# Optimization experiments

Measured on AMD Instinct MI355X. Metric: run time of the kernel, lower is better.

## Reference

```python
import jax, jax.numpy as jnp
import numpy as np

H = 12        # heads
D = 768       # d_model
DK = D // H   # per-head dim
B, S = 1, 4096


def setup_inputs() -> dict:
    key = jax.random.key(0)
    ks = jax.random.split(key, 8)
    scale = 1.0 / np.sqrt(D)
    return {
        "q": jax.random.normal(ks[0], (B, S, D), jnp.float32),
        "k": jax.random.normal(ks[1], (B, S, D), jnp.float32),
        "v": jax.random.normal(ks[2], (B, S, D), jnp.float32),
        "Wq": jax.random.normal(ks[3], (D, D), jnp.float32) * scale,
        "bq": jnp.zeros((D,), jnp.float32),
        "Wk": jax.random.normal(ks[4], (D, D), jnp.float32) * scale,
        "bk": jnp.zeros((D,), jnp.float32),
        "Wv": jax.random.normal(ks[5], (D, D), jnp.float32) * scale,
        "bv": jnp.zeros((D,), jnp.float32),
        "Wo": jax.random.normal(ks[6], (D, D), jnp.float32) * scale,
        "bo": jnp.zeros((D,), jnp.float32),
    }


def reference(q, k, v, Wq, bq, Wk, bk, Wv, bv, Wo, bo):
    bs, sq, _ = q.shape
    sk = k.shape[1]
    # projections, then split heads: (b, h, s, dk)
    qh = (q @ Wq + bq).reshape(bs, sq, H, DK).transpose(0, 2, 1, 3)
    kh = (k @ Wk + bk).reshape(bs, sk, H, DK).transpose(0, 2, 1, 3)
    vh = (v @ Wv + bv).reshape(bs, sk, H, DK).transpose(0, 2, 1, 3)
    # scaled dot-product attention (mask=None, dropout inactive)
    scores = jnp.einsum("bhqd,bhkd->bhqk", qh, kh) / jnp.sqrt(jnp.float32(DK))
    attn = jax.nn.softmax(scores, axis=-1)
    ctx = jnp.einsum("bhqk,bhkd->bhqd", attn, vh)
    concat = ctx.transpose(0, 2, 1, 3).reshape(bs, sq, D)
    return concat @ Wo + bo
```

## Files before the change

### kernel.cpp

```cpp
#include <hip/hip_runtime.h>
#include <hip/hip_bf16.h>


constexpr int S_LEN = 4096;
constexpr int D_MODEL = 768;
constexpr int N_HEADS = 12;
constexpr int D_HEAD = 64;
constexpr int SEG = 2;
constexpr int SEG_LEN = S_LEN / SEG;

#define QSCALE 0.180336880111120f

typedef _Float16 f16;
typedef __attribute__((ext_vector_type(8))) _Float16 f16x8;
typedef __attribute__((ext_vector_type(4))) _Float16 f16x4;
typedef __attribute__((ext_vector_type(4))) float f32x4;

__global__ __launch_bounds__(256) void prep_kernel(
    const float* __restrict__ q, const float* __restrict__ k,
    const float* __restrict__ v, f16* __restrict__ qh,
    f16* __restrict__ kh, f16* __restrict__ vh,
    const float* __restrict__ W0, const float* __restrict__ W1,
    const float* __restrict__ W2, const float* __restrict__ W3,
    f16* __restrict__ WtBase)
{
    __shared__ float T[64][65];
    int bid = blockIdx.x;
    const int t = threadIdx.x;
    if (bid < 4608) {
        int g = bid / 1536, r = bid % 1536;
        const float* x = (g == 0) ? q : (g == 1) ? k : v;
        f16* y = (g == 0) ? qh : (g == 1) ? kh : vh;
        int i = (r * 256 + t) * 8;
        float4 a = *(const float4*)&x[i];
        float4 b = *(const float4*)&x[i + 4];
        f16x8 h = { (f16)a.x, (f16)a.y, (f16)a.z, (f16)a.w,
                    (f16)b.x, (f16)b.y, (f16)b.z, (f16)b.w };
        *(f16x8*)&y[i] = h;
        return;
    }
    bid -= 4608;
    int g = bid / 144, r = bid % 144;
    const float* W = (g == 0) ? W0 : (g == 1) ? W1 : (g == 2) ? W2 : W3;
    f16* Wt = WtBase + (size_t)g * D_MODEL * D_MODEL;
    const int r0 = (r / 12) * 64;
    const int c0 = (r % 12) * 64;
    #pragma unroll
    for (int i = 0; i < 16; ++i) {
        int e = t + 256 * i; int rr = e >> 6, cc = e & 63;
        T[rr][cc] = W[(size_t)(r0 + rr) * D_MODEL + c0 + cc];
    }
    __syncthreads();
    #pragma unroll
    for (int i = 0; i < 16; ++i) {
        int e = t + 256 * i; int rr = e >> 6, cc = e & 63;
        Wt[(size_t)(c0 + rr) * D_MODEL + r0 + cc] = (f16)T[cc][rr];
    }
}

#define GSTR 72

__device__ __forceinline__ void gemm128_core(
    const f16* __restrict__ A, const f16* __restrict__ B,
    f16* As, f16* Bs, int K, int row0, int col0, int t, f32x4 acc[4][4])
{
    const int w = t >> 6, l = t & 63, quad = l >> 4, l15 = l & 15;
    const int wm = (w & 1) * 64, wn = (w >> 1) * 64;

    f16x8 pa[4], pb[4];
    #pragma unroll
    for (int i = 0; i < 4; ++i) {
        int idx = i * 256 + t;
        int r = idx >> 3, c = (idx & 7) * 8;
        pa[i] = *(const f16x8*)&A[(size_t)(row0 + r) * K + c];
        pb[i] = *(const f16x8*)&B[(size_t)(col0 + r) * K + c];
    }

    for (int k0 = 0; k0 < K; k0 += 64) {
        __syncthreads();
        #pragma unroll
        for (int i = 0; i < 4; ++i) {
            int idx = i * 256 + t;
            int r = idx >> 3, c = (idx & 7) * 8;
            *(f16x8*)&As[r * GSTR + c] = pa[i];
            *(f16x8*)&Bs[r * GSTR + c] = pb[i];
        }
        __syncthreads();

        int kn = k0 + 64;
        if (kn < K) {
            #pragma unroll
            for (int i = 0; i < 4; ++i) {
                int idx = i * 256 + t;
                int r = idx >> 3, c = (idx & 7) * 8;
                pa[i] = *(const f16x8*)&A[(size_t)(row0 + r) * K + kn + c];
                pb[i] = *(const f16x8*)&B[(size_t)(col0 + r) * K + kn + c];
            }
        }

        #pragma unroll
        for (int kc = 0; kc < 2; ++kc) {
            f16x8 af[4], bf[4];
            #pragma unroll
            for (int mt = 0; mt < 4; ++mt)
                af[mt] = *(f16x8*)&As[(wm + mt * 16 + l15) * GSTR + kc * 32 + quad * 8];
            #pragma unroll
            for (int nt = 0; nt < 4; ++nt)
                bf[nt] = *(f16x8*)&Bs[(wn + nt * 16 + l15) * GSTR + kc * 32 + quad * 8];
            #pragma unroll
            for (int mt = 0; mt < 4; ++mt)
                #pragma unroll
                for (int nt = 0; nt < 4; ++nt)
                    acc[mt][nt] = __builtin_amdgcn_mfma_f32_16x16x32_f16(
                        af[mt], bf[nt], acc[mt][nt], 0, 0, 0);
        }
    }
}

__global__ __launch_bounds__(256) void qkv_gemm_kernel(
    const f16* __restrict__ qh, const f16* __restrict__ kh,
    const f16* __restrict__ vh, const f16* __restrict__ WtBase,
    const float* __restrict__ bq, const float* __restrict__ bk,
    const float* __restrict__ bv,
    f16* __restrict__ Qp, f16* __restrict__ Kp, f16* __restrict__ Vpt)
{
    __shared__ f16 As[128 * GSTR];
    __shared__ f16 Bs[128 * GSTR];
    const size_t DD = (size_t)D_MODEL * D_MODEL;
    int bid = blockIdx.x;
    int g = bid / 192, r = bid % 192;

    const f16 *A, *B; const float* bias; f16* Y;
    int N; bool biasRow; float scale;
    int row0, col0;
    if (g == 0) {
        A = qh; B = WtBase; bias = bq; Y = Qp;
        N = D_MODEL; biasRow = false; scale = QSCALE;
        row0 = (r / 6) * 128; col0 = (r % 6) * 128;
    } else if (g == 1) {
        A = kh; B = WtBase + DD; bias = bk; Y = Kp;
        N = D_MODEL; biasRow = false; scale = 1.0f;
        row0 = (r / 6) * 128; col0 = (r % 6) * 128;
    } else {
        A = WtBase + 2 * DD; B = vh; bias = bv; Y = Vpt;
        N = S_LEN; biasRow = true; scale = 1.0f;
        row0 = (r / 32) * 128; col0 = (r % 32) * 128;
    }

    f32x4 acc[4][4];
    #pragma unroll
    for (int i = 0; i < 4; ++i)
        #pragma unroll
        for (int j = 0; j < 4; ++j) acc[i][j] = (f32x4){0.f, 0.f, 0.f, 0.f};

    const int t = threadIdx.x;
    gemm128_core(A, B, As, Bs, D_MODEL, row0, col0, t, acc);

    const int w = t >> 6, l = t & 63, quad = l >> 4, l15 = l & 15;
    const int wm = (w & 1) * 64, wn = (w >> 1) * 64;
    #pragma unroll
    for (int mt = 0; mt < 4; ++mt) {
        #pragma unroll
        for (int nt = 0; nt < 4; ++nt) {
            int col = col0 + wn + nt * 16 + l15;
            #pragma unroll
            for (int reg = 0; reg < 4; ++reg) {
                int row = row0 + wm + mt * 16 + quad * 4 + reg;
                float b = biasRow ? bias[row] : bias[col];
                Y[(size_t)row * N + col] = (f16)((acc[mt][nt][reg] + b) * scale);
            }
        }
    }
}

#define LSTR 72

__global__ __launch_bounds__(256, 4) void flash_attn_part_kernel(
    const f16* __restrict__ Q, const f16* __restrict__ K,
    const f16* __restrict__ Vg, f16* __restrict__ Opart,
    float* __restrict__ lsum)
{
    __shared__ f16 Ks[64 * LSTR];
    __shared__ f16 Vt[64 * LSTR];

    const int t    = threadIdx.x;
    const int w    = t >> 6;
    const int l    = t & 63;
    const int quad = l >> 4;
    const int l15  = l & 15;
    const int h    = blockIdx.y;
    const int q0   = blockIdx.x * 128;
    const int seg  = blockIdx.z;
    const int c0   = h * D_HEAD;
    const size_t SD = (size_t)S_LEN * D_MODEL;

    f16x8 qa[2][2];
    #pragma unroll
    for (int qt = 0; qt < 2; ++qt) {
        const f16* qrow = Q + (size_t)(q0 + w * 32 + qt * 16 + l15) * D_MODEL + c0;
        qa[qt][0] = *(const f16x8*)&qrow[quad * 8];
        qa[qt][1] = *(const f16x8*)&qrow[32 + quad * 8];
    }

    f32x4 ctx[2][4];
    float lAcc[2] = {0.f, 0.f};
    #pragma unroll
    for (int qt = 0; qt < 2; ++qt)
        #pragma unroll
        for (int i = 0; i < 4; ++i) ctx[qt][i] = (f32x4){0.f, 0.f, 0.f, 0.f};

    const int kt0 = seg * SEG_LEN;

    f16x8 kreg[2], vreg[2];
    #pragma unroll
    for (int i = 0; i < 2; ++i) {
        int idx = i * 256 + t;
        int r = idx >> 3, c = (idx & 7) * 8;
        kreg[i] = *(const f16x8*)&K[(size_t)(kt0 + r) * D_MODEL + c0 + c];
        vreg[i] = *(const f16x8*)&Vg[(size_t)(c0 + r) * S_LEN + kt0 + c];
    }

    for (int kt = kt0; kt < kt0 + SEG_LEN; kt += 64) {
        __syncthreads();
        #pragma unroll
        for (int i = 0; i < 2; ++i) {
            int idx = i * 256 + t;
            int r = idx >> 3, c = (idx & 7) * 8;
            *(f16x8*)&Ks[r * LSTR + c] = kreg[i];
            *(f16x8*)&Vt[r * LSTR + c] = vreg[i];
        }
        __syncthreads();

        int ktn = kt + 64;
        if (ktn < kt0 + SEG_LEN) {
            #pragma unroll
            for (int i = 0; i < 2; ++i) {
                int idx = i * 256 + t;
                int r = idx >> 3, c = (idx & 7) * 8;
                kreg[i] = *(const f16x8*)&K[(size_t)(ktn + r) * D_MODEL + c0 + c];
                vreg[i] = *(const f16x8*)&Vg[(size_t)(c0 + r) * S_LEN + ktn + c];
            }
        }

        f16x4 pfrag[2][4];
        #pragma unroll
        for (int nt = 0; nt < 4; ++nt) {
            f16x8 kb0 = *(f16x8*)&Ks[(nt * 16 + l15) * LSTR + quad * 8];
            f16x8 kb1 = *(f16x8*)&Ks[(nt * 16 + l15) * LSTR + 32 + quad * 8];
            #pragma unroll
            for (int qt = 0; qt < 2; ++qt) {
                f32x4 z = (f32x4){0.f, 0.f, 0.f, 0.f};
                z = __builtin_amdgcn_mfma_f32_16x16x32_f16(kb0, qa[qt][0], z, 0, 0, 0);
                z = __builtin_amdgcn_mfma_f32_16x16x32_f16(kb1, qa[qt][1], z, 0, 0, 0);
                float p0 = __builtin_amdgcn_exp2f(z[0]);
                float p1 = __builtin_amdgcn_exp2f(z[1]);
                float p2 = __builtin_amdgcn_exp2f(z[2]);
                float p3 = __builtin_amdgcn_exp2f(z[3]);
                lAcc[qt] += (p0 + p1) + (p2 + p3);
                pfrag[qt][nt] = (f16x4){ (f16)p0, (f16)p1, (f16)p2, (f16)p3 };
            }
        }

        #pragma unroll
        for (int mt = 0; mt < 4; ++mt) {
            #pragma unroll
            for (int nt = 0; nt < 4; ++nt) {
                f16x4 va = *(f16x4*)&Vt[(mt * 16 + l15) * LSTR + nt * 16 + quad * 4];
                #pragma unroll
                for (int qt = 0; qt < 2; ++qt)
                    ctx[qt][mt] = __builtin_amdgcn_mfma_f32_16x16x16f16(
                        va, pfrag[qt][nt], ctx[qt][mt], 0, 0, 0);
            }
        }
    }

    #pragma unroll
    for (int qt = 0; qt < 2; ++qt) {
        int qrow = q0 + w * 32 + qt * 16 + l15;
        #pragma unroll
        for (int mt = 0; mt < 4; ++mt) {
            f16x4 ov = { (f16)ctx[qt][mt][0], (f16)ctx[qt][mt][1],
                         (f16)ctx[qt][mt][2], (f16)ctx[qt][mt][3] };
            *(f16x4*)&Opart[(size_t)seg * SD + (size_t)qrow * D_MODEL
                            + c0 + mt * 16 + quad * 4] = ov;
        }
        float s = lAcc[qt];
        s += __shfl_xor(s, 16);
        s += __shfl_xor(s, 32);
        if (quad == 0)
            lsum[((size_t)seg * N_HEADS + h) * S_LEN + qrow] = s;
    }
}

__global__ __launch_bounds__(256) void combine_kernel(
    const f16* __restrict__ Opart, const float* __restrict__ lsum,
    f16* __restrict__ Ctx)
{
    const size_t SD = (size_t)S_LEN * D_MODEL;
    int tid = blockIdx.x * 256 + threadIdx.x;
    int idx = tid * 8;
    int row = idx / D_MODEL;
    int c   = idx % D_MODEL;
    int h   = c >> 6;
    float l0 = lsum[(size_t)h * S_LEN + row];
    float l1 = lsum[((size_t)N_HEADS + h) * S_LEN + row];
    float inv = 1.0f / (l0 + l1);
    f16x8 o0 = *(const f16x8*)&Opart[(size_t)row * D_MODEL + c];
    f16x8 o1 = *(const f16x8*)&Opart[SD + (size_t)row * D_MODEL + c];
    f16x8 r;
    #pragma unroll
    for (int j = 0; j < 8; ++j)
        r[j] = (f16)(((float)o0[j] + (float)o1[j]) * inv);
    *(f16x8*)&Ctx[(size_t)row * D_MODEL + c] = r;
}

__global__ __launch_bounds__(256) void oproj_kernel(
    const f16* __restrict__ Ctx, const f16* __restrict__ Wto,
    const float* __restrict__ bo, float* __restrict__ out)
{
    __shared__ f16 As[128 * GSTR];
    __shared__ f16 Bs[128 * GSTR];
    int bid = blockIdx.x;
    int row0 = (bid / 6) * 128, col0 = (bid % 6) * 128;

    f32x4 acc[4][4];
    #pragma unroll
    for (int i = 0; i < 4; ++i)
        #pragma unroll
        for (int j = 0; j < 4; ++j) acc[i][j] = (f32x4){0.f, 0.f, 0.f, 0.f};

    const int t = threadIdx.x;
    gemm128_core(Ctx, Wto, As, Bs, D_MODEL, row0, col0, t, acc);

    const int w = t >> 6, l = t & 63, quad = l >> 4, l15 = l & 15;
    const int wm = (w & 1) * 64, wn = (w >> 1) * 64;
    #pragma unroll
    for (int mt = 0; mt < 4; ++mt) {
        #pragma unroll
        for (int nt = 0; nt < 4; ++nt) {
            int col = col0 + wn + nt * 16 + l15;
            float b = bo[col];
            #pragma unroll
            for (int reg = 0; reg < 4; ++reg) {
                int row = row0 + wm + mt * 16 + quad * 4 + reg;
                out[(size_t)row * D_MODEL + col] = acc[mt][nt][reg] + b;
            }
        }
    }
}

extern "C" void kernel_launch(void* const* d_in, const int* in_sizes, int n_in,
                              void* d_out, int out_size, void* d_ws, size_t ws_size,
                              hipStream_t stream)
{
    const float* q  = (const float*)d_in[0];
    const float* k  = (const float*)d_in[1];
    const float* v  = (const float*)d_in[2];
    const float* Wq = (const float*)d_in[3];
    const float* bq = (const float*)d_in[4];
    const float* Wk = (const float*)d_in[5];
    const float* bk = (const float*)d_in[6];
    const float* Wv = (const float*)d_in[7];
    const float* bv = (const float*)d_in[8];
    const float* Wo = (const float*)d_in[9];
    const float* bo = (const float*)d_in[10];
    float* out = (float*)d_out;

    const size_t SD = (size_t)S_LEN * D_MODEL;
    const size_t DD = (size_t)D_MODEL * D_MODEL;
    f16* base   = (f16*)d_ws;
    f16* WtBase = base;
    f16* Wto    = WtBase + 3 * DD;
    f16* Qp     = base + 4 * DD;
    f16* Kp     = Qp + SD;
    f16* Vpt    = Kp + SD;
    f16* qh     = Vpt + SD;
    f16* kh     = qh + SD;
    f16* vh     = kh + SD;
    f16* Opart  = qh;
    f16* Ctx    = qh + 2 * SD;
    float* lsum = (float*)(base + 4 * DD + 6 * SD);

    prep_kernel<<<3 * 1536 + 4 * 144, 256, 0, stream>>>(
        q, k, v, qh, kh, vh, Wq, Wk, Wv, Wo, WtBase);

    qkv_gemm_kernel<<<3 * 192, 256, 0, stream>>>(
        qh, kh, vh, WtBase, bq, bk, bv, Qp, Kp, Vpt);

    dim3 gAttn(S_LEN / 128, N_HEADS, SEG);
    flash_attn_part_kernel<<<gAttn, 256, 0, stream>>>(Qp, Kp, Vpt, Opart, lsum);

    combine_kernel<<<1536, 256, 0, stream>>>(Opart, lsum, Ctx);

    oproj_kernel<<<192, 256, 0, stream>>>(Ctx, Wto, bo, out);
}
```

Before: 224.7 us.

## Load GEMM tiles directly to LDS with XOR swizzle instead of register staging

Changes the shared GEMM core used by the QKV and output projections. Tiles now go straight from global memory into LDS with global_load_lds, replacing the register prefetch followed by an LDS store. The padded row stride becomes a dense 64-wide layout with an XOR chunk swizzle to avoid bank conflicts. This frees registers and LDS space, but removes the software prefetch overlap: every iteration now waits on the load before its MFMAs run.

```diff
diff --git a/kernel.cpp b/kernel.cpp
--- a/kernel.cpp
+++ b/kernel.cpp
@@ -15,6 +15,13 @@
 typedef __attribute__((ext_vector_type(8))) _Float16 f16x8;
 typedef __attribute__((ext_vector_type(4))) _Float16 f16x4;
 typedef __attribute__((ext_vector_type(4))) float f32x4;
+
+__device__ __forceinline__ void cp16(const f16* gsrc, f16* ldsbase_uniform) {
+    __builtin_amdgcn_global_load_lds(
+        (__attribute__((address_space(1))) void*)(uintptr_t)gsrc,
+        (__attribute__((address_space(3))) void*)(uintptr_t)ldsbase_uniform,
+        16, 0, 0);
+}
 
 __global__ __launch_bounds__(256) void prep_kernel(
     const float* __restrict__ q, const float* __restrict__ k,
@@ -58,55 +65,38 @@
     }
 }
 
-#define GSTR 72
-
 __device__ __forceinline__ void gemm128_core(
     const f16* __restrict__ A, const f16* __restrict__ B,
     f16* As, f16* Bs, int K, int row0, int col0, int t, f32x4 acc[4][4])
 {
     const int w = t >> 6, l = t & 63, quad = l >> 4, l15 = l & 15;
     const int wm = (w & 1) * 64, wn = (w >> 1) * 64;
-
-    f16x8 pa[4], pb[4];
-    #pragma unroll
-    for (int i = 0; i < 4; ++i) {
-        int idx = i * 256 + t;
-        int r = idx >> 3, c = (idx & 7) * 8;
-        pa[i] = *(const f16x8*)&A[(size_t)(row0 + r) * K + c];
-        pb[i] = *(const f16x8*)&B[(size_t)(col0 + r) * K + c];
-    }
+    const int srow   = l >> 3;
+    const int gchunk = (l & 7) ^ srow;
+    const int swz    = l15 & 7;
 
     for (int k0 = 0; k0 < K; k0 += 64) {
         __syncthreads();
         #pragma unroll
-        for (int i = 0; i < 4; ++i) {
-            int idx = i * 256 + t;
-            int r = idx >> 3, c = (idx & 7) * 8;
-            *(f16x8*)&As[r * GSTR + c] = pa[i];
-            *(f16x8*)&Bs[r * GSTR + c] = pb[i];
+        for (int j = 0; j < 4; ++j) {
+            int m = w * 4 + j;
+            int r = m * 8 + srow;
+            cp16(&A[(size_t)(row0 + r) * K + k0 + gchunk * 8], &As[m * 512]);
+            cp16(&B[(size_t)(col0 + r) * K + k0 + gchunk * 8], &Bs[m * 512]);
         }
         __syncthreads();
-
-        int kn = k0 + 64;
-        if (kn < K) {
-            #pragma unroll
-            for (int i = 0; i < 4; ++i) {
-                int idx = i * 256 + t;
-                int r = idx >> 3, c = (idx & 7) * 8;
-                pa[i] = *(const f16x8*)&A[(size_t)(row0 + r) * K + kn + c];
-                pb[i] = *(const f16x8*)&B[(size_t)(col0 + r) * K + kn + c];
-            }
-        }
 
         #pragma unroll
         for (int kc = 0; kc < 2; ++kc) {
             f16x8 af[4], bf[4];
             #pragma unroll
             for (int mt = 0; mt < 4; ++mt)
-                af[mt] = *(f16x8*)&As[(wm + mt * 16 + l15) * GSTR + kc * 32 + quad * 8];
+                af[mt] = *(f16x8*)&As[(wm + mt * 16 + l15) * 64
+                                      + (((kc * 4 + quad) ^ swz) * 8)];
             #pragma unroll
             for (int nt = 0; nt < 4; ++nt)
-                bf[nt] = *(f16x8*)&Bs[(wn + nt * 16 + l15) * GSTR + kc * 32 + quad * 8];
+                bf[nt] = *(f16x8*)&Bs[(wn + nt * 16 + l15) * 64
+                                      + (((kc * 4 + quad) ^ swz) * 8)];
             #pragma unroll
             for (int mt = 0; mt < 4; ++mt)
                 #pragma unroll
@@ -124,8 +114,8 @@
     const float* __restrict__ bv,
     f16* __restrict__ Qp, f16* __restrict__ Kp, f16* __restrict__ Vpt)
 {
-    __shared__ f16 As[128 * GSTR];
-    __shared__ f16 Bs[128 * GSTR];
+    __shared__ f16 As[128 * 64];
+    __shared__ f16 Bs[128 * 64];
     const size_t DD = (size_t)D_MODEL * D_MODEL;
     int bid = blockIdx.x;
     int g = bid / 192, r = bid % 192;
@@ -318,8 +308,8 @@
     const f16* __restrict__ Ctx, const f16* __restrict__ Wto,
     const float* __restrict__ bo, float* __restrict__ out)
 {
-    __shared__ f16 As[128 * GSTR];
-    __shared__ f16 Bs[128 * GSTR];
+    __shared__ f16 As[128 * 64];
+    __shared__ f16 Bs[128 * 64];
     int bid = blockIdx.x;
     int row0 = (bid / 6) * 128, col0 = (bid % 6) * 128;
 
```

Measured after the change: 232.2 us. 1.03x slower.

## Split attention KV into four segments and halve GEMM N-tile width

Applied to the files above, without the earlier changes.

Raises the flash-attention KV split from 2 to 4 segments, so the grid has more blocks, and generalizes the combine kernel to sum an arbitrary number of partials. The QKV and output-projection GEMMs move from 128x128 to 128x64 tiles through a templated core, doubling block counts for better occupancy across the CUs. The workspace layout changes: Ctx now aliases Qp and lsum moves to make room for four Opart buffers. The trade-off is more partial-output traffic in combine and less operand reuse per GEMM tile.

```diff
diff --git a/kernel.cpp b/kernel.cpp
--- a/kernel.cpp
+++ b/kernel.cpp
@@ -6,7 +6,7 @@
 constexpr int D_MODEL = 768;
 constexpr int N_HEADS = 12;
 constexpr int D_HEAD = 64;
-constexpr int SEG = 2;
+constexpr int SEG = 4;
 constexpr int SEG_LEN = S_LEN / SEG;
 
 #define QSCALE 0.180336880111120f
@@ -60,19 +60,25 @@
 
 #define GSTR 72
 
-__device__ __forceinline__ void gemm128_core(
+template<int NT>
+__device__ __forceinline__ void gemm_core(
     const f16* __restrict__ A, const f16* __restrict__ B,
-    f16* As, f16* Bs, int K, int row0, int col0, int t, f32x4 acc[4][4])
+    f16* As, f16* Bs, int K, int row0, int col0, int t, f32x4 acc[4][NT])
 {
     const int w = t >> 6, l = t & 63, quad = l >> 4, l15 = l & 15;
-    const int wm = (w & 1) * 64, wn = (w >> 1) * 64;
-
-    f16x8 pa[4], pb[4];
+    const int wm = (w & 1) * 64, wn = (w >> 1) * 16 * NT;
+
+    f16x8 pa[4], pb[NT];
     #pragma unroll
     for (int i = 0; i < 4; ++i) {
         int idx = i * 256 + t;
         int r = idx >> 3, c = (idx & 7) * 8;
         pa[i] = *(const f16x8*)&A[(size_t)(row0 + r) * K + c];
+    }
+    #pragma unroll
+    for (int i = 0; i < NT; ++i) {
+        int idx = i * 256 + t;
+        int r = idx >> 3, c = (idx & 7) * 8;
         pb[i] = *(const f16x8*)&B[(size_t)(col0 + r) * K + c];
     }
 
@@ -83,6 +89,11 @@
             int idx = i * 256 + t;
             int r = idx >> 3, c = (idx & 7) * 8;
             *(f16x8*)&As[r * GSTR + c] = pa[i];
+        }
+        #pragma unroll
+        for (int i = 0; i < NT; ++i) {
+            int idx = i * 256 + t;
+            int r = idx >> 3, c = (idx & 7) * 8;
             *(f16x8*)&Bs[r * GSTR + c] = pb[i];
         }
         __syncthreads();
@@ -94,23 +105,28 @@
                 int idx = i * 256 + t;
                 int r = idx >> 3, c = (idx & 7) * 8;
                 pa[i] = *(const f16x8*)&A[(size_t)(row0 + r) * K + kn + c];
+            }
+            #pragma unroll
+            for (int i = 0; i < NT; ++i) {
+                int idx = i * 256 + t;
+                int r = idx >> 3, c = (idx & 7) * 8;
                 pb[i] = *(const f16x8*)&B[(size_t)(col0 + r) * K + kn + c];
             }
         }
 
         #pragma unroll
         for (int kc = 0; kc < 2; ++kc) {
-            f16x8 af[4], bf[4];
+            f16x8 af[4], bf[NT];
             #pragma unroll
             for (int mt = 0; mt < 4; ++mt)
                 af[mt] = *(f16x8*)&As[(wm + mt * 16 + l15) * GSTR + kc * 32 + quad * 8];
             #pragma unroll
-            for (int nt = 0; nt < 4; ++nt)
+            for (int nt = 0; nt < NT; ++nt)
                 bf[nt] = *(f16x8*)&Bs[(wn + nt * 16 + l15) * GSTR + kc * 32 + quad * 8];
             #pragma unroll
             for (int mt = 0; mt < 4; ++mt)
                 #pragma unroll
-                for (int nt = 0; nt < 4; ++nt)
+                for (int nt = 0; nt < NT; ++nt)
                     acc[mt][nt] = __builtin_amdgcn_mfma_f32_16x16x32_f16(
                         af[mt], bf[nt], acc[mt][nt], 0, 0, 0);
         }
@@ -125,10 +141,10 @@
     f16* __restrict__ Qp, f16* __restrict__ Kp, f16* __restrict__ Vpt)
 {
     __shared__ f16 As[128 * GSTR];
-    __shared__ f16 Bs[128 * GSTR];
+    __shared__ f16 Bs[64 * GSTR];
     const size_t DD = (size_t)D_MODEL * D_MODEL;
     int bid = blockIdx.x;
-    int g = bid / 192, r = bid % 192;
+    int g = bid / 384, r = bid % 384;
 
     const f16 *A, *B; const float* bias; f16* Y;
     int N; bool biasRow; float scale;
@@ -136,32 +152,32 @@
     if (g == 0) {
         A = qh; B = WtBase; bias = bq; Y = Qp;
         N = D_MODEL; biasRow = false; scale = QSCALE;
-        row0 = (r / 6) * 128; col0 = (r % 6) * 128;
+        row0 = (r / 12) * 128; col0 = (r % 12) * 64;
     } else if (g == 1) {
         A = kh; B = WtBase + DD; bias = bk; Y = Kp;
         N = D_MODEL; biasRow = false; scale = 1.0f;
-        row0 = (r / 6) * 128; col0 = (r % 6) * 128;
+        row0 = (r / 12) * 128; col0 = (r % 12) * 64;
     } else {
         A = WtBase + 2 * DD; B = vh; bias = bv; Y = Vpt;
         N = S_LEN; biasRow = true; scale = 1.0f;
-        row0 = (r / 32) * 128; col0 = (r % 32) * 128;
-    }
-
-    f32x4 acc[4][4];
+        row0 = (r / 64) * 128; col0 = (r % 64) * 64;
+    }
+
+    f32x4 acc[4][2];
     #pragma unroll
     for (int i = 0; i < 4; ++i)
         #pragma unroll
-        for (int j = 0; j < 4; ++j) acc[i][j] = (f32x4){0.f, 0.f, 0.f, 0.f};
+        for (int j = 0; j < 2; ++j) acc[i][j] = (f32x4){0.f, 0.f, 0.f, 0.f};
 
     const int t = threadIdx.x;
-    gemm128_core(A, B, As, Bs, D_MODEL, row0, col0, t, acc);
+    gemm_core<2>(A, B, As, Bs, D_MODEL, row0, col0, t, acc);
 
     const int w = t >> 6, l = t & 63, quad = l >> 4, l15 = l & 15;
-    const int wm = (w & 1) * 64, wn = (w >> 1) * 64;
+    const int wm = (w & 1) * 64, wn = (w >> 1) * 32;
     #pragma unroll
     for (int mt = 0; mt < 4; ++mt) {
         #pragma unroll
-        for (int nt = 0; nt < 4; ++nt) {
+        for (int nt = 0; nt < 2; ++nt) {
             int col = col0 + wn + nt * 16 + l15;
             #pragma unroll
             for (int reg = 0; reg < 4; ++reg) {
@@ -302,15 +318,21 @@
     int row = idx / D_MODEL;
     int c   = idx % D_MODEL;
     int h   = c >> 6;
-    float l0 = lsum[(size_t)h * S_LEN + row];
-    float l1 = lsum[((size_t)N_HEADS + h) * S_LEN + row];
-    float inv = 1.0f / (l0 + l1);
-    f16x8 o0 = *(const f16x8*)&Opart[(size_t)row * D_MODEL + c];
-    f16x8 o1 = *(const f16x8*)&Opart[SD + (size_t)row * D_MODEL + c];
+    float lt = 0.f;
+    #pragma unroll
+    for (int s = 0; s < SEG; ++s)
+        lt += lsum[((size_t)s * N_HEADS + h) * S_LEN + row];
+    float inv = 1.0f / lt;
+    float o[8] = {};
+    #pragma unroll
+    for (int s = 0; s < SEG; ++s) {
+        f16x8 ov = *(const f16x8*)&Opart[(size_t)s * SD + (size_t)row * D_MODEL + c];
+        #pragma unroll
+        for (int j = 0; j < 8; ++j) o[j] += (float)ov[j];
+    }
     f16x8 r;
     #pragma unroll
-    for (int j = 0; j < 8; ++j)
-        r[j] = (f16)(((float)o0[j] + (float)o1[j]) * inv);
+    for (int j = 0; j < 8; ++j) r[j] = (f16)(o[j] * inv);
     *(f16x8*)&Ctx[(size_t)row * D_MODEL + c] = r;
 }
 
@@ -319,25 +341,25 @@
     const float* __restrict__ bo, float* __restrict__ out)
 {
     __shared__ f16 As[128 * GSTR];
-    __shared__ f16 Bs[128 * GSTR];
+    __shared__ f16 Bs[64 * GSTR];
     int bid = blockIdx.x;
-    int row0 = (bid / 6) * 128, col0 = (bid % 6) * 128;
-
-    f32x4 acc[4][4];
+    int row0 = (bid / 12) * 128, col0 = (bid % 12) * 64;
+
+    f32x4 acc[4][2];
     #pragma unroll
     for (int i = 0; i < 4; ++i)
         #pragma unroll
-        for (int j = 0; j < 4; ++j) acc[i][j] = (f32x4){0.f, 0.f, 0.f, 0.f};
+        for (int j = 0; j < 2; ++j) acc[i][j] = (f32x4){0.f, 0.f, 0.f, 0.f};
 
     const int t = threadIdx.x;
-    gemm128_core(Ctx, Wto, As, Bs, D_MODEL, row0, col0, t, acc);
+    gemm_core<2>(Ctx, Wto, As, Bs, D_MODEL, row0, col0, t, acc);
 
     const int w = t >> 6, l = t & 63, quad = l >> 4, l15 = l & 15;
-    const int wm = (w & 1) * 64, wn = (w >> 1) * 64;
+    const int wm = (w & 1) * 64, wn = (w >> 1) * 32;
     #pragma unroll
     for (int mt = 0; mt < 4; ++mt) {
         #pragma unroll
-        for (int nt = 0; nt < 4; ++nt) {
+        for (int nt = 0; nt < 2; ++nt) {
             int col = col0 + wn + nt * 16 + l15;
             float b = bo[col];
             #pragma unroll
@@ -378,13 +400,13 @@
     f16* kh     = qh + SD;
     f16* vh     = kh + SD;
     f16* Opart  = qh;
-    f16* Ctx    = qh + 2 * SD;
-    float* lsum = (float*)(base + 4 * DD + 6 * SD);
+    float* lsum = (float*)(base + 4 * DD + 7 * SD);
+    f16* Ctx    = Qp;
 
     prep_kernel<<<3 * 1536 + 4 * 144, 256, 0, stream>>>(
         q, k, v, qh, kh, vh, Wq, Wk, Wv, Wo, WtBase);
 
-    qkv_gemm_kernel<<<3 * 192, 256, 0, stream>>>(
+    qkv_gemm_kernel<<<3 * 384, 256, 0, stream>>>(
         qh, kh, vh, WtBase, bq, bk, bv, Qp, Kp, Vpt);
 
     dim3 gAttn(S_LEN / 128, N_HEADS, SEG);
@@ -392,5 +414,5 @@
 
     combine_kernel<<<1536, 256, 0, stream>>>(Opart, lsum, Ctx);
 
-    oproj_kernel<<<192, 256, 0, stream>>>(Ctx, Wto, bo, out);
-}
+    oproj_kernel<<<384, 256, 0, stream>>>(Ctx, Wto, bo, out);
+}
```

Result: slower. 230.5 us (+2.6%).

## Double-buffer attention K/V via direct global-to-LDS loads and split keys into four segments

Applied to the files above, without the earlier changes.

Replaces the register-staged K/V tile loading in the flash attention kernel with async global_load_lds copies into double-buffered, XOR-swizzled LDS tiles, removing one barrier per iteration and the register round trip. The key dimension is now split into 4 segments instead of 2, doubling the grid for more parallelism, and the combine kernel is generalized to sum over all segments. Workspace layout shifts so Opart spans four SD slices, Ctx reuses the Qp buffer, and lsum moves further out. Trade-offs are more partial-output traffic in combine and reliance on the swizzle matching the lane-to-LDS mapping of the direct loads.

```diff
diff --git a/kernel.cpp b/kernel.cpp
--- a/kernel.cpp
+++ b/kernel.cpp
@@ -6,8 +6,9 @@
 constexpr int D_MODEL = 768;
 constexpr int N_HEADS = 12;
 constexpr int D_HEAD = 64;
-constexpr int SEG = 2;
+constexpr int SEG = 4;
 constexpr int SEG_LEN = S_LEN / SEG;
+constexpr int NITER = SEG_LEN / 64;
 
 #define QSCALE 0.180336880111120f
 
@@ -15,6 +16,13 @@
 typedef __attribute__((ext_vector_type(8))) _Float16 f16x8;
 typedef __attribute__((ext_vector_type(4))) _Float16 f16x4;
 typedef __attribute__((ext_vector_type(4))) float f32x4;
+
+__device__ __forceinline__ void cp16(const f16* gsrc, f16* ldsbase_uniform) {
+    __builtin_amdgcn_global_load_lds(
+        (__attribute__((address_space(1))) void*)(uintptr_t)gsrc,
+        (__attribute__((address_space(3))) void*)(uintptr_t)ldsbase_uniform,
+        16, 0, 0);
+}
 
 __global__ __launch_bounds__(256) void prep_kernel(
     const float* __restrict__ q, const float* __restrict__ k,
@@ -173,15 +181,13 @@
     }
 }
 
-#define LSTR 72
-
 __global__ __launch_bounds__(256, 4) void flash_attn_part_kernel(
     const f16* __restrict__ Q, const f16* __restrict__ K,
     const f16* __restrict__ Vg, f16* __restrict__ Opart,
     float* __restrict__ lsum)
 {
-    __shared__ f16 Ks[64 * LSTR];
-    __shared__ f16 Vt[64 * LSTR];
+    __shared__ f16 Ks[2][64 * 64];
+    __shared__ f16 Vt[2][64 * 64];
 
     const int t    = threadIdx.x;
     const int w    = t >> 6;
@@ -194,6 +200,10 @@
     const int c0   = h * D_HEAD;
     const size_t SD = (size_t)S_LEN * D_MODEL;
 
+    const int swz = l15 & 7;
+    const int lr  = l >> 3;
+    const int gch = (l & 7) ^ lr;
+
     f16x8 qa[2][2];
     #pragma unroll
     for (int qt = 0; qt < 2; ++qt) {
@@ -211,42 +221,32 @@
 
     const int kt0 = seg * SEG_LEN;
 
-    f16x8 kreg[2], vreg[2];
-    #pragma unroll
-    for (int i = 0; i < 2; ++i) {
-        int idx = i * 256 + t;
-        int r = idx >> 3, c = (idx & 7) * 8;
-        kreg[i] = *(const f16x8*)&K[(size_t)(kt0 + r) * D_MODEL + c0 + c];
-        vreg[i] = *(const f16x8*)&Vg[(size_t)(c0 + r) * S_LEN + kt0 + c];
-    }
-
-    for (int kt = kt0; kt < kt0 + SEG_LEN; kt += 64) {
-        __syncthreads();
-        #pragma unroll
-        for (int i = 0; i < 2; ++i) {
-            int idx = i * 256 + t;
-            int r = idx >> 3, c = (idx & 7) * 8;
-            *(f16x8*)&Ks[r * LSTR + c] = kreg[i];
-            *(f16x8*)&Vt[r * LSTR + c] = vreg[i];
-        }
-        __syncthreads();
-
-        int ktn = kt + 64;
-        if (ktn < kt0 + SEG_LEN) {
-            #pragma unroll
-            for (int i = 0; i < 2; ++i) {
-                int idx = i * 256 + t;
-                int r = idx >> 3, c = (idx & 7) * 8;
-                kreg[i] = *(const f16x8*)&K[(size_t)(ktn + r) * D_MODEL + c0 + c];
-                vreg[i] = *(const f16x8*)&Vg[(size_t)(c0 + r) * S_LEN + ktn + c];
-            }
-        }
+    auto stage = [&](int buf, int kt) {
+        #pragma unroll
+        for (int j = 0; j < 2; ++j) {
+            int rbase = w * 16 + j * 8;
+            cp16(&K[(size_t)(kt + rbase + lr) * D_MODEL + c0 + gch * 8],
+                 &Ks[buf][rbase * 64]);
+            cp16(&Vg[(size_t)(c0 + rbase + lr) * S_LEN + kt + gch * 8],
+                 &Vt[buf][rbase * 64]);
+        }
+    };
+
+    stage(0, kt0);
+    __syncthreads();
+
+    for (int it = 0; it < NITER; ++it) {
+        const int buf = it & 1;
+        if (it + 1 < NITER) stage(1 - buf, kt0 + (it + 1) * 64);
+
+        const f16* ks = Ks[buf];
+        const f16* vt = Vt[buf];
 
         f16x4 pfrag[2][4];
         #pragma unroll
         for (int nt = 0; nt < 4; ++nt) {
-            f16x8 kb0 = *(f16x8*)&Ks[(nt * 16 + l15) * LSTR + quad * 8];
-            f16x8 kb1 = *(f16x8*)&Ks[(nt * 16 + l15) * LSTR + 32 + quad * 8];
+            f16x8 kb0 = *(const f16x8*)&ks[(nt * 16 + l15) * 64 + ((quad ^ swz) * 8)];
+            f16x8 kb1 = *(const f16x8*)&ks[(nt * 16 + l15) * 64 + (((4 + quad) ^ swz) * 8)];
             #pragma unroll
             for (int qt = 0; qt < 2; ++qt) {
                 f32x4 z = (f32x4){0.f, 0.f, 0.f, 0.f};
@@ -265,13 +265,16 @@
         for (int mt = 0; mt < 4; ++mt) {
             #pragma unroll
             for (int nt = 0; nt < 4; ++nt) {
-                f16x4 va = *(f16x4*)&Vt[(mt * 16 + l15) * LSTR + nt * 16 + quad * 4];
+                f16x4 va = *(const f16x4*)&vt[(mt * 16 + l15) * 64
+                    + (((2 * nt + (quad >> 1)) ^ swz) * 8) + (quad & 1) * 4];
                 #pragma unroll
                 for (int qt = 0; qt < 2; ++qt)
                     ctx[qt][mt] = __builtin_amdgcn_mfma_f32_16x16x16f16(
                         va, pfrag[qt][nt], ctx[qt][mt], 0, 0, 0);
             }
         }
+
+        __syncthreads();
     }
 
     #pragma unroll
@@ -302,15 +305,21 @@
     int row = idx / D_MODEL;
     int c   = idx % D_MODEL;
     int h   = c >> 6;
-    float l0 = lsum[(size_t)h * S_LEN + row];
-    float l1 = lsum[((size_t)N_HEADS + h) * S_LEN + row];
-    float inv = 1.0f / (l0 + l1);
-    f16x8 o0 = *(const f16x8*)&Opart[(size_t)row * D_MODEL + c];
-    f16x8 o1 = *(const f16x8*)&Opart[SD + (size_t)row * D_MODEL + c];
+    float lt = 0.f;
+    #pragma unroll
+    for (int s = 0; s < SEG; ++s)
+        lt += lsum[((size_t)s * N_HEADS + h) * S_LEN + row];
+    float inv = 1.0f / lt;
+    float o[8] = {};
+    #pragma unroll
+    for (int s = 0; s < SEG; ++s) {
+        f16x8 ov = *(const f16x8*)&Opart[(size_t)s * SD + (size_t)row * D_MODEL + c];
+        #pragma unroll
+        for (int j = 0; j < 8; ++j) o[j] += (float)ov[j];
+    }
     f16x8 r;
     #pragma unroll
-    for (int j = 0; j < 8; ++j)
-        r[j] = (f16)(((float)o0[j] + (float)o1[j]) * inv);
+    for (int j = 0; j < 8; ++j) r[j] = (f16)(o[j] * inv);
     *(f16x8*)&Ctx[(size_t)row * D_MODEL + c] = r;
 }
 
@@ -378,8 +387,8 @@
     f16* kh     = qh + SD;
     f16* vh     = kh + SD;
     f16* Opart  = qh;
-    f16* Ctx    = qh + 2 * SD;
-    float* lsum = (float*)(base + 4 * DD + 6 * SD);
+    float* lsum = (float*)(base + 4 * DD + 7 * SD);
+    f16* Ctx    = Qp;
 
     prep_kernel<<<3 * 1536 + 4 * 144, 256, 0, stream>>>(
         q, k, v, qh, kh, vh, Wq, Wk, Wv, Wo, WtBase);
```

Result: no change. 224.9 us (+0.1%).
